# Kernel tuning notes

Hardware: AMD Instinct MI355X
Metric: run time of the kernel (lower is better)

Reference implementation:

```python
import jax, jax.numpy as jnp
import numpy as np

K_NEIGHBORS = 6
LN_EPS = 1e-5


def _layernorm(h, g, b):
    m = h.mean(-1, keepdims=True)
    v = h.var(-1, keepdims=True)
    return (h - m) / jnp.sqrt(v + LN_EPS) * g + b


def _mlp(h, w0, b0, w1, b1):
    return jax.nn.relu(h @ w0 + b0) @ w1 + b1


def _learn_adj(x, Wp, bp):
    # EfficientGraphStructureLearner: cosine-sim topk graph, symmetrized, row-normalized
    h = x @ Wp + bp
    nrm = jnp.linalg.norm(h, axis=1, keepdims=True)
    h = h / jnp.maximum(nrm, 1e-12)
    S = h @ h.T                                  # [N, N]
    vals, idx = jax.lax.top_k(S, K_NEIGHBORS + 1)  # col 0 is self (diag == 1)
    N = x.shape[0]
    rows = jnp.arange(N)[:, None]
    adj = jnp.zeros_like(S).at[rows, idx[:, 1:]].set(vals[:, 1:])
    adj = (adj + adj.T) * 0.5
    adj = adj / (adj.sum(1, keepdims=True) + 1e-8)
    return adj


def _gcn(h, adj, W, b):
    # StandardGraphConv: D^-1/2 (A+I) D^-1/2 @ (h W) + b (diag matmuls as row/col scaling)
    A = adj + jnp.eye(adj.shape[0], dtype=adj.dtype)
    d = jnp.maximum(A.sum(1), 1e-12) ** -0.5
    norm_adj = d[:, None] * A * d[None, :]
    return norm_adj @ (h @ W) + b


def setup_inputs() -> dict:
    key = jax.random.key(0)
    ks = iter(jax.random.split(key, 40))
    N, D, H, O, HP = 8192, 20, 32, 128, 16
    f = lambda *s: jax.random.normal(next(ks), s, dtype=jnp.float32) * 0.1
    inp = {
        'x': jax.random.normal(next(ks), (N, D), dtype=jnp.float32),
        'Wp': f(D, HP), 'bp': jnp.zeros((HP,), jnp.float32),
        'gw0': f(D, H), 'gb0': jnp.zeros((H,), jnp.float32),
        'gw1': f(H, H), 'gb1': jnp.zeros((H,), jnp.float32),
        'gw2': f(H, O), 'gb2': jnp.zeros((O,), jnp.float32),
        'lg0': jnp.ones((H,), jnp.float32), 'lb0': jnp.zeros((H,), jnp.float32),
        'lg1': jnp.ones((H,), jnp.float32), 'lb1': jnp.zeros((H,), jnp.float32),
        'lg2': jnp.ones((O,), jnp.float32), 'lb2': jnp.zeros((O,), jnp.float32),
        'riw0': f(D, H), 'rib0': jnp.zeros((H,), jnp.float32),
        'riw1': f(H, H), 'rib1': jnp.zeros((H,), jnp.float32),
        'rhw0': f(H, H), 'rhb0': jnp.zeros((H,), jnp.float32),
        'rhw1': f(H, H), 'rhb1': jnp.zeros((H,), jnp.float32),
        'row0': f(H, O), 'rob0': jnp.zeros((O,), jnp.float32),
        'row1': f(O, O), 'rob1': jnp.zeros((O,), jnp.float32),
    }
    return inp


def reference(x, Wp, bp, gw0, gb0, gw1, gb1, gw2, gb2,
              lg0, lb0, lg1, lb1, lg2, lb2,
              riw0, rib0, riw1, rib1,
              rhw0, rhb0, rhw1, rhb1,
              row0, rob0, row1, rob1):
    adj = _learn_adj(x, Wp, bp)
    gcns = [(gw0, gb0, lg0, lb0), (gw1, gb1, lg1, lb1), (gw2, gb2, lg2, lb2)]
    skips = [(riw0, rib0, riw1, rib1), (rhw0, rhb0, rhw1, rhb1), (row0, rob0, row1, rob1)]
    h = x
    for i, ((W, b, g, bt), sk) in enumerate(zip(gcns, skips)):
        h_new = jax.nn.relu(_layernorm(_gcn(h, adj, W, b), g, bt))
        h = h_new + _mlp(h, *sk)
        # dropout is identity in eval mode
    return h
```

## Files before the change

### kernel.cpp

```cpp
#include <hip/hip_runtime.h>

constexpr int D_IN = 20;
constexpr int HP   = 16;
constexpr int K    = 6;
constexpr int SAMP = 512;
constexpr int NC   = 8;
constexpr int CAPC = 192;
constexpr int CIN  = 128;
constexpr float MARGIN = 0.02f;

typedef __attribute__((ext_vector_type(8))) short bf16x8;
typedef __attribute__((ext_vector_type(4))) float f32x4;

__device__ __forceinline__ float dot16_seq(const float4* q, const float4* c) {
  float s = 0.f;
#pragma unroll
  for (int m = 0; m < 4; ++m) {
    s = fmaf(q[m].x, c[m].x, s);
    s = fmaf(q[m].y, c[m].y, s);
    s = fmaf(q[m].z, c[m].z, s);
    s = fmaf(q[m].w, c[m].w, s);
  }
  return s;
}

__device__ __forceinline__ short f2bf(float f) {
  unsigned u = __float_as_uint(f);
  unsigned r = (u + 0x7fffu + ((u >> 16) & 1u)) >> 16;
  return (short)r;
}

__device__ __forceinline__ float dinv_of(float own, float ins) {
  float rs = 0.5f * (own + ins);
  float rn = 1.f / (rs + 1e-8f);
  return rsqrtf(fmaxf(1.f + rs * rn, 1e-12f));
}

__global__ void k_proj(const float* __restrict__ x, const float* __restrict__ Wp,
                       const float* __restrict__ bp, const float* __restrict__ gw0,
                       float* __restrict__ hn, short* __restrict__ hnb,
                       float* __restrict__ XW0,
                       float* __restrict__ insum, int* __restrict__ indeg, int N) {
  int i = blockIdx.x * blockDim.x + threadIdx.x;
  if (i >= N) return;
  insum[i] = 0.f; indeg[i] = 0;
  float xr[D_IN];
#pragma unroll
  for (int d = 0; d < D_IN; ++d) xr[d] = x[i*D_IN + d];
  float hv[HP];
  float nrm2 = 0.f;
#pragma unroll
  for (int h = 0; h < HP; ++h) {
    float a = bp[h];
#pragma unroll
    for (int d = 0; d < D_IN; ++d) a += xr[d] * Wp[d*HP + h];
    hv[h] = a;
    nrm2 += a * a;
  }
  float inv = 1.f / fmaxf(sqrtf(nrm2), 1e-12f);
#pragma unroll
  for (int h = 0; h < HP; ++h) {
    float v = hv[h] * inv;
    hn[i*HP + h] = v;
    hnb[(size_t)i*32 + h] = f2bf(v);
  }
#pragma unroll
  for (int h = 0; h < HP; ++h) hnb[(size_t)i*32 + 16 + h] = 0;
#pragma unroll
  for (int oc = 0; oc < 32; ++oc) {
    float a = 0.f;
#pragma unroll
    for (int d = 0; d < D_IN; ++d) a += xr[d] * gw0[d*32 + oc];
    XW0[(size_t)i*32 + oc] = a;
  }
}

struct Top6 { float v0,v1,v2,v3,v4,v5; int i0,i1,i2,i3,i4,i5; };

__device__ __forceinline__ void t6_init(Top6& t) {
  t.v0=t.v1=t.v2=t.v3=t.v4=t.v5=-1e30f;
  t.i0=t.i1=t.i2=t.i3=t.i4=t.i5=-1;
}

#define T6_SWAP(a,b,ia,ib) { float tv=a; a=b; b=tv; int ti=ia; ia=ib; ib=ti; }

__device__ __forceinline__ void t6_insert(Top6& t, float s, int c) {
  if (s > t.v5) {
    t.v5 = s; t.i5 = c;
    if (t.v5 > t.v4) { T6_SWAP(t.v4, t.v5, t.i4, t.i5); }
    if (t.v4 > t.v3) { T6_SWAP(t.v3, t.v4, t.i3, t.i4); }
    if (t.v3 > t.v2) { T6_SWAP(t.v2, t.v3, t.i2, t.i3); }
    if (t.v2 > t.v1) { T6_SWAP(t.v1, t.v2, t.i1, t.i2); }
    if (t.v1 > t.v0) { T6_SWAP(t.v0, t.v1, t.i0, t.i1); }
  }
}

__device__ __forceinline__ void t6_best(const Top6& t, float& cv, int& ci) {
  cv = t.v0; ci = t.i0;
  if (t.v1 > cv || (t.v1 == cv && (unsigned)t.i1 < (unsigned)ci)) { cv = t.v1; ci = t.i1; }
  if (t.v2 > cv || (t.v2 == cv && (unsigned)t.i2 < (unsigned)ci)) { cv = t.v2; ci = t.i2; }
  if (t.v3 > cv || (t.v3 == cv && (unsigned)t.i3 < (unsigned)ci)) { cv = t.v3; ci = t.i3; }
  if (t.v4 > cv || (t.v4 == cv && (unsigned)t.i4 < (unsigned)ci)) { cv = t.v4; ci = t.i4; }
  if (t.v5 > cv || (t.v5 == cv && (unsigned)t.i5 < (unsigned)ci)) { cv = t.v5; ci = t.i5; }
}

__device__ __forceinline__ void t6_consume(Top6& t, int mi) {
  if (t.i0 == mi) t.v0 = -1e30f;
  if (t.i1 == mi) t.v1 = -1e30f;
  if (t.i2 == mi) t.v2 = -1e30f;
  if (t.i3 == mi) t.v3 = -1e30f;
  if (t.i4 == mi) t.v4 = -1e30f;
  if (t.i5 == mi) t.v5 = -1e30f;
}

__global__ __launch_bounds__(256) void k_thresh(const float* __restrict__ hn,
                                                float* __restrict__ tau, int N) {
  int wave = threadIdx.x >> 6, lane = threadIdx.x & 63;
  int row = blockIdx.x * 4 + wave;
  const float4* hn4 = (const float4*)hn;
  float4 q[4];
#pragma unroll
  for (int m = 0; m < 4; ++m) q[m] = hn4[(size_t)row*4 + m];
  Top6 t; t6_init(t);
#pragma unroll
  for (int k = 0; k < SAMP/64; ++k) {
    int c = lane + 64*k;
    if (c != row) {
      float4 cv[4];
#pragma unroll
      for (int m = 0; m < 4; ++m) cv[m] = hn4[(size_t)c*4 + m];
      float s = dot16_seq(q, cv);
      t6_insert(t, s, c);
    }
  }
  float last = -1e30f;
  for (int sel = 0; sel < K; ++sel) {
    float cv; int ci;
    t6_best(t, cv, ci);
    float mv = cv; int mi = ci;
#pragma unroll
    for (int m = 1; m < 64; m <<= 1) {
      float ov = __shfl_xor(mv, m);
      int   oi = __shfl_xor(mi, m);
      if (ov > mv || (ov == mv && (unsigned)oi < (unsigned)mi)) { mv = ov; mi = oi; }
    }
    t6_consume(t, mi);
    last = mv;
  }
  if (lane == 0) tau[row] = last;
}

__global__ __launch_bounds__(256) void k_scan2(
    const short* __restrict__ hnb, const float* __restrict__ tau,
    int* __restrict__ cnt, unsigned short* __restrict__ buf, int N) {
  __shared__ int cntl[16];
  int rb = blockIdx.x / NC;
  int jc = blockIdx.x % NC;
  int wave = threadIdx.x >> 6, lane = threadIdx.x & 63;
  int r0 = rb * 16;
  int half = lane >> 4;
  int l16  = lane & 15;

  if (threadIdx.x < 16) cntl[threadIdx.x] = 0;
  __syncthreads();

  bf16x8 a = *(const bf16x8*)(hnb + (size_t)(r0 + l16)*32 + half*8);
  float4 t4 = *(const float4*)(tau + r0 + half*4);
  float tm0 = t4.x - MARGIN, tm1 = t4.y - MARGIN,
        tm2 = t4.z - MARGIN, tm3 = t4.w - MARGIN;
  f32x4 zero = {0.f, 0.f, 0.f, 0.f};

  const int SPANW = N / NC / 4;
  int jb0 = jc * (N / NC) + wave * SPANW;

#define APPB(R, COND)                                                        \
  {                                                                          \
    unsigned long long mr = __ballot(COND);                                  \
    if (l16 == 0) {                                                          \
      unsigned mask = (unsigned)(mr >> (16*half)) & 0xFFFFu;                 \
      if (mask) {                                                            \
        int row = r0 + half*4 + (R);                                         \
        int pos = atomicAdd(&cntl[4*half + (R)], __popc(mask));              \
        unsigned mm = mask;                                                  \
        while (mm) {                                                         \
          int bx = __ffs(mm) - 1; mm &= mm - 1;                              \
          if (pos < CAPC)                                                    \
            buf[((size_t)row*NC + jc)*CAPC + pos] = (unsigned short)(jb + bx); \
          ++pos;                                                             \
        }                                                                    \
      }                                                                      \
    }                                                                        \
  }

#pragma unroll 4
  for (int jt = 0; jt < SPANW; jt += 16) {
    int jb = jb0 + jt;
    bf16x8 b = *(const bf16x8*)(hnb + (size_t)(jb + l16)*32 + half*8);
    f32x4 d = __builtin_amdgcn_mfma_f32_16x16x32_bf16(a, b, zero, 0, 0, 0);
    bool h0 = d[0] >= tm0, h1 = d[1] >= tm1, h2 = d[2] >= tm2, h3 = d[3] >= tm3;
    if (__any(h0 | h1 | h2 | h3)) {
      APPB(0, h0) APPB(1, h1) APPB(2, h2) APPB(3, h3)
    }
  }
#undef APPB

  __syncthreads();
  if (threadIdx.x < 16)
    cnt[(size_t)(r0 + threadIdx.x)*NC + jc] = min(cntl[threadIdx.x], CAPC);
}

__global__ __launch_bounds__(256) void k_final(
    const float* __restrict__ hn, const unsigned short* __restrict__ buf,
    const int* __restrict__ cnt,
    float* __restrict__ evals, int* __restrict__ eidx,
    float* __restrict__ ownsum, float* insum, int* indeg,
    unsigned short* __restrict__ incol, float* __restrict__ inval, int N) {
  int wave = threadIdx.x >> 6, lane = threadIdx.x & 63;
  int row = blockIdx.x * 4 + wave;
  const float4* hn4 = (const float4*)hn;
  float4 q[4];
#pragma unroll
  for (int m = 0; m < 4; ++m) q[m] = hn4[(size_t)row*4 + m];

  int cbase = row * NC;
  int cl = (lane < NC) ? cnt[cbase + lane] : 0;
  int c0 = __shfl(cl, 0), c1 = __shfl(cl, 1), c2 = __shfl(cl, 2), c3 = __shfl(cl, 3),
      c4 = __shfl(cl, 4), c5 = __shfl(cl, 5), c6 = __shfl(cl, 6), c7 = __shfl(cl, 7);
  int p1 = c0, p2 = p1 + c1, p3 = p2 + c2, p4 = p3 + c3,
      p5 = p4 + c4, p6 = p5 + c5, p7 = p6 + c6, T = p7 + c7;

  Top6 t; t6_init(t);
  for (int e = lane; e < T; e += 64) {
    int s, off;
    if (e < p4) {
      if (e < p2) { if (e < p1) { s = 0; off = e; } else { s = 1; off = e - p1; } }
      else        { if (e < p3) { s = 2; off = e - p2; } else { s = 3; off = e - p3; } }
    } else {
      if (e < p6) { if (e < p5) { s = 4; off = e - p4; } else { s = 5; off = e - p5; } }
      else        { if (e < p7) { s = 6; off = e - p6; } else { s = 7; off = e - p7; } }
    }
    int j = buf[((size_t)cbase + s)*CAPC + off];
    if (j != row) {
      float4 cv[4];
#pragma unroll
      for (int m = 0; m < 4; ++m) cv[m] = hn4[(size_t)j*4 + m];
      float sc = dot16_seq(q, cv);
      t6_insert(t, sc, j);
    }
  }
  float osum = 0.f;
  for (int sel = 0; sel < K; ++sel) {
    float cv; int ci;
    t6_best(t, cv, ci);
    float mv = cv; int mi = ci;
#pragma unroll
    for (int m = 1; m < 64; m <<= 1) {
      float ov = __shfl_xor(mv, m);
      int   oi = __shfl_xor(mi, m);
      if (ov > mv || (ov == mv && (unsigned)oi < (unsigned)mi)) { mv = ov; mi = oi; }
    }
    t6_consume(t, mi);
    if (lane == 0) {
      evals[row*K + sel] = mv;
      eidx [row*K + sel] = mi;
      osum += mv;
      atomicAdd(&insum[mi], mv);
      int pos = atomicAdd(&indeg[mi], 1);
      if (pos < CIN) {
        incol[(size_t)mi*CIN + pos] = (unsigned short)row;
        inval[(size_t)mi*CIN + pos] = mv;
      }
    }
  }
  if (lane == 0) ownsum[row] = osum;
}

template<int DIN, int NEXTD>
__global__ __launch_bounds__(256) void k_gpost32(
    const float* __restrict__ XWsrc,
    const int* __restrict__ eidx, const float* __restrict__ evals,
    const unsigned short* __restrict__ incol, const float* __restrict__ inval,
    const int* __restrict__ indeg,
    const float* __restrict__ ownsum, const float* __restrict__ insum,
    const float* __restrict__ gb, const float* __restrict__ lg, const float* __restrict__ lb,
    const float* __restrict__ hprev,
    const float* __restrict__ w0, const float* __restrict__ b0,
    const float* __restrict__ w1, const float* __restrict__ b1,
    const float* __restrict__ Wnext, float* __restrict__ XWnext,
    float* __restrict__ outp, int N) {
  __shared__ float hid[4][2][32];
  int tid = threadIdx.x;
  int lane = tid & 63, wslot = tid >> 6;
  int sub = lane >> 5, ol = lane & 31;
  int row = (blockIdx.x * 4 + wslot) * 2 + sub;

  float rs_i = 0.5f * (ownsum[row] + insum[row]);
  float rn_i = 1.f / (rs_i + 1e-8f);
  float di_i = rsqrtf(fmaxf(1.f + rs_i * rn_i, 1e-12f));
  float cc = 0.5f * di_i * rn_i;
  float acc = (di_i * di_i) * XWsrc[(size_t)row*32 + ol];
#pragma unroll
  for (int t = 0; t < K; ++t) {
    int j = eidx[row*K + t]; float v = evals[row*K + t];
    float dj = dinv_of(ownsum[j], insum[j]);
    acc = fmaf(cc * v * dj, XWsrc[(size_t)j*32 + ol], acc);
  }
  int ne = min(indeg[row], CIN);
  for (int e = 0; e < ne; ++e) {
    int j = incol[(size_t)row*CIN + e]; float v = inval[(size_t)row*CIN + e];
    float dj = dinv_of(ownsum[j], insum[j]);
    acc = fmaf(cc * v * dj, XWsrc[(size_t)j*32 + ol], acc);
  }
  float u0 = acc + gb[ol];
  float s = u0;
#pragma unroll
  for (int m = 1; m < 32; m <<= 1) s += __shfl_xor(s, m);
  float mean = s * (1.f/32.f);
  float d0 = u0 - mean;
  float vs = d0*d0;
#pragma unroll
  for (int m = 1; m < 32; m <<= 1) vs += __shfl_xor(vs, m);
  float rstd = rsqrtf(vs * (1.f/32.f) + 1e-5f);
  float t0 = fmaxf(d0*rstd*lg[ol] + lb[ol], 0.f);

  float hp[DIN];
#pragma unroll
  for (int d = 0; d < DIN; ++d) hp[d] = hprev[(size_t)row*DIN + d];
  float a = b0[ol];
#pragma unroll
  for (int d = 0; d < DIN; ++d) a = fmaf(hp[d], w0[d*32 + ol], a);
  hid[wslot][sub][ol] = fmaxf(a, 0.f);
  float o = b1[ol];
#pragma unroll
  for (int h = 0; h < 32; ++h) o = fmaf(hid[wslot][sub][h], w1[h*32 + ol], o);
  float hv = t0 + o;
  outp[(size_t)row*32 + ol] = hv;

  hid[wslot][sub][ol] = hv;
#pragma unroll
  for (int k2 = 0; k2 < NEXTD/32; ++k2) {
    int oc = ol + 32*k2;
    float acc2 = 0.f;
#pragma unroll
    for (int d = 0; d < 32; ++d)
      acc2 = fmaf(hid[wslot][sub][d], Wnext[d*NEXTD + oc], acc2);
    XWnext[(size_t)row*NEXTD + oc] = acc2;
  }
}

__global__ __launch_bounds__(256) void k_gpost128(
    const float* __restrict__ XW,
    const int* __restrict__ eidx, const float* __restrict__ evals,
    const unsigned short* __restrict__ incol, const float* __restrict__ inval,
    const int* __restrict__ indeg,
    const float* __restrict__ ownsum, const float* __restrict__ insum,
    const float* __restrict__ b, const float* __restrict__ g, const float* __restrict__ bt,
    const float* __restrict__ hprev,
    const float* __restrict__ w0, const float* __restrict__ b0,
    const float* __restrict__ w1, const float* __restrict__ b1,
    float* __restrict__ out, int N) {
  __shared__ float hid_s[4][128];
  __shared__ float w1s[2048];
  int wslot = threadIdx.x >> 6;
  int row   = (blockIdx.x * blockDim.x + threadIdx.x) >> 6;
  int lane  = threadIdx.x & 63;
  int o0 = lane, o1 = lane + 64;

  float rs_i = 0.5f * (ownsum[row] + insum[row]);
  float rn_i = 1.f / (rs_i + 1e-8f);
  float di_i = rsqrtf(fmaxf(1.f + rs_i * rn_i, 1e-12f));
  float cc = 0.5f * di_i * rn_i;
  float sc = di_i * di_i;
  float acc0 = sc * XW[(size_t)row*128 + o0];
  float acc1 = sc * XW[(size_t)row*128 + o1];
#pragma unroll
  for (int t = 0; t < K; ++t) {
    int j = eidx[row*K + t]; float v = evals[row*K + t];
    float dj = dinv_of(ownsum[j], insum[j]);
    float cf = cc * v * dj;
    acc0 = fmaf(cf, XW[(size_t)j*128 + o0], acc0);
    acc1 = fmaf(cf, XW[(size_t)j*128 + o1], acc1);
  }
  int ne = min(indeg[row], CIN);
  for (int e = 0; e < ne; ++e) {
    int j = incol[(size_t)row*CIN + e]; float v = inval[(size_t)row*CIN + e];
    float dj = dinv_of(ownsum[j], insum[j]);
    float cf = cc * v * dj;
    acc0 = fmaf(cf, XW[(size_t)j*128 + o0], acc0);
    acc1 = fmaf(cf, XW[(size_t)j*128 + o1], acc1);
  }
  float u0 = acc0 + b[o0];
  float u1 = acc1 + b[o1];

  float s = u0 + u1;
#pragma unroll
  for (int m = 1; m < 64; m <<= 1) s += __shfl_xor(s, m);
  float mean = s * (1.f/128.f);
  float d0 = u0 - mean, d1 = u1 - mean;
  float vs = d0*d0 + d1*d1;
#pragma unroll
  for (int m = 1; m < 64; m <<= 1) vs += __shfl_xor(vs, m);
  float rstd = rsqrtf(vs * (1.f/128.f) + 1e-5f);
  float t0 = fmaxf(d0*rstd*g[o0] + bt[o0], 0.f);
  float t1 = fmaxf(d1*rstd*g[o1] + bt[o1], 0.f);

  float hp[32];
#pragma unroll
  for (int d = 0; d < 32; ++d) hp[d] = hprev[(size_t)row*32 + d];
  {
    float a = b0[o0];
#pragma unroll
    for (int d = 0; d < 32; ++d) a = fmaf(hp[d], w0[d*128 + o0], a);
    hid_s[wslot][o0] = fmaxf(a, 0.f);
    float a1 = b0[o1];
#pragma unroll
    for (int d = 0; d < 32; ++d) a1 = fmaf(hp[d], w0[d*128 + o1], a1);
    hid_s[wslot][o1] = fmaxf(a1, 0.f);
  }

  float r0=0.f, r1=0.f, r2=0.f, r3=0.f, q0=0.f, q1=0.f, q2=0.f, q3=0.f;
  for (int c = 0; c < 8; ++c) {
    __syncthreads();
    {
      const float4* src = (const float4*)(w1 + c*2048);
      float4* dst = (float4*)w1s;
      dst[threadIdx.x]       = src[threadIdx.x];
      dst[threadIdx.x + 256] = src[threadIdx.x + 256];
    }
    __syncthreads();
    int hb = c*16;
#pragma unroll
    for (int hh = 0; hh < 16; hh += 4) {
      float h0 = hid_s[wslot][hb+hh+0], h1 = hid_s[wslot][hb+hh+1],
            h2 = hid_s[wslot][hb+hh+2], h3 = hid_s[wslot][hb+hh+3];
      r0 = fmaf(h0, w1s[(hh+0)*128 + o0], r0); q0 = fmaf(h0, w1s[(hh+0)*128 + o1], q0);
      r1 = fmaf(h1, w1s[(hh+1)*128 + o0], r1); q1 = fmaf(h1, w1s[(hh+1)*128 + o1], q1);
      r2 = fmaf(h2, w1s[(hh+2)*128 + o0], r2); q2 = fmaf(h2, w1s[(hh+2)*128 + o1], q2);
      r3 = fmaf(h3, w1s[(hh+3)*128 + o0], r3); q3 = fmaf(h3, w1s[(hh+3)*128 + o1], q3);
    }
  }
  out[(size_t)row*128 + o0] = t0 + b1[o0] + ((r0 + r1) + (r2 + r3));
  out[(size_t)row*128 + o1] = t1 + b1[o1] + ((q0 + q1) + (q2 + q3));
}

extern "C" void kernel_launch(void* const* d_in, const int* in_sizes, int n_in,
                              void* d_out, int out_size, void* d_ws, size_t ws_size,
                              hipStream_t stream) {
  const float* x    = (const float*)d_in[0];
  const float* Wp   = (const float*)d_in[1];
  const float* bp   = (const float*)d_in[2];
  const float* gw0  = (const float*)d_in[3];
  const float* gb0  = (const float*)d_in[4];
  const float* gw1  = (const float*)d_in[5];
  const float* gb1  = (const float*)d_in[6];
  const float* gw2  = (const float*)d_in[7];
  const float* gb2  = (const float*)d_in[8];
  const float* lg0  = (const float*)d_in[9];
  const float* lb0  = (const float*)d_in[10];
  const float* lg1  = (const float*)d_in[11];
  const float* lb1  = (const float*)d_in[12];
  const float* lg2  = (const float*)d_in[13];
  const float* lb2  = (const float*)d_in[14];
  const float* riw0 = (const float*)d_in[15];
  const float* rib0 = (const float*)d_in[16];
  const float* riw1 = (const float*)d_in[17];
  const float* rib1 = (const float*)d_in[18];
  const float* rhw0 = (const float*)d_in[19];
  const float* rhb0 = (const float*)d_in[20];
  const float* rhw1 = (const float*)d_in[21];
  const float* rhb1 = (const float*)d_in[22];
  const float* row0 = (const float*)d_in[23];
  const float* rob0 = (const float*)d_in[24];
  const float* row1 = (const float*)d_in[25];
  const float* rob1 = (const float*)d_in[26];
  int N = in_sizes[0] / D_IN;
  float* out = (float*)d_out;

  char* ws = (char*)d_ws;
  size_t off = 0;
  auto alloc = [&](size_t bytes) -> void* {
    void* p = ws + off;
    off += (bytes + 255) & ~(size_t)255;
    return p;
  };
  float* hn      = (float*)alloc((size_t)N * HP * 4);
  float* evals   = (float*)alloc((size_t)N * K * 4);
  int*   eidx    = (int*)  alloc((size_t)N * K * 4);
  float* ownsum  = (float*)alloc((size_t)N * 4);
  float* insum   = (float*)alloc((size_t)N * 4);
  int*   indeg   = (int*)  alloc((size_t)N * 4);
  float* XWa     = (float*)alloc((size_t)N * 128 * 4);
  float* XWb     = (float*)alloc((size_t)N * 32 * 4);
  float* h1      = (float*)alloc((size_t)N * 32 * 4);
  float* h2      = (float*)alloc((size_t)N * 32 * 4);
  float* tau     = (float*)alloc((size_t)N * 4);
  int*   cnt     = (int*)  alloc((size_t)N * NC * 4);
  unsigned short* buf = (unsigned short*)alloc((size_t)N * NC * CAPC * 2);
  short* hnb     = (short*)alloc((size_t)N * 32 * 2);
  unsigned short* incol = (unsigned short*)alloc((size_t)N * CIN * 2);
  float* inval   = (float*)alloc((size_t)N * CIN * 4);
  (void)ws_size; (void)n_in; (void)out_size;

  const int B = 256;
  hipLaunchKernelGGL(k_proj, dim3((N + B - 1) / B), dim3(B), 0, stream,
                     x, Wp, bp, gw0, hn, hnb, XWa, insum, indeg, N);
  hipLaunchKernelGGL(k_thresh, dim3(N / 4), dim3(B), 0, stream, hn, tau, N);
  hipLaunchKernelGGL(k_scan2, dim3((N / 16) * NC), dim3(B), 0, stream, hnb, tau, cnt, buf, N);
  hipLaunchKernelGGL(k_final, dim3(N / 4), dim3(B), 0, stream,
                     hn, buf, cnt, evals, eidx, ownsum, insum, indeg, incol, inval, N);

  hipLaunchKernelGGL((k_gpost32<20, 32>), dim3(N / 8), dim3(B), 0, stream,
                     XWa, eidx, evals, incol, inval, indeg, ownsum, insum,
                     gb0, lg0, lb0, x, riw0, rib0, riw1, rib1, gw1, XWb, h1, N);
  hipLaunchKernelGGL((k_gpost32<32, 128>), dim3(N / 8), dim3(B), 0, stream,
                     XWb, eidx, evals, incol, inval, indeg, ownsum, insum,
                     gb1, lg1, lb1, h1, rhw0, rhb0, rhw1, rhb1, gw2, XWa, h2, N);
  hipLaunchKernelGGL(k_gpost128, dim3(N / 4), dim3(B), 0, stream,
                     XWa, eidx, evals, incol, inval, indeg, ownsum, insum,
                     gb2, lg2, lb2, h2, row0, rob0, row1, rob1, out, N);
}
```

Measured before the change: 153.9 us.

## Fuse threshold sampling into projection kernel and pre-scale XW by degree

The separate threshold kernel is folded into the projection kernel. Each thread now computes its 6th-best cosine similarity against the 256 rows of its own block, read from shared memory, instead of a wave-wide top-6 over 512 sampled rows, which removes one launch and a global reload of hn. Separately, each row's XW output is pre-multiplied by its own D^-1/2 factor, so the second and third GCN aggregations no longer gather ownsum and insum for every neighbour. The threshold sample changes (its own block's 256 rows instead of the first 512 rows, and per-thread instead of per-wave), which may shift the candidate counts in the scan buffers and their overflow behaviour.

```diff
diff --git a/kernel.cpp b/kernel.cpp
--- a/kernel.cpp
+++ b/kernel.cpp
@@ -3,7 +3,6 @@
 constexpr int D_IN = 20;
 constexpr int HP   = 16;
 constexpr int K    = 6;
-constexpr int SAMP = 512;
 constexpr int NC   = 8;
 constexpr int CAPC = 192;
 constexpr int CIN  = 128;
@@ -34,45 +33,6 @@
   float rs = 0.5f * (own + ins);
   float rn = 1.f / (rs + 1e-8f);
   return rsqrtf(fmaxf(1.f + rs * rn, 1e-12f));
-}
-
-__global__ void k_proj(const float* __restrict__ x, const float* __restrict__ Wp,
-                       const float* __restrict__ bp, const float* __restrict__ gw0,
-                       float* __restrict__ hn, short* __restrict__ hnb,
-                       float* __restrict__ XW0,
-                       float* __restrict__ insum, int* __restrict__ indeg, int N) {
-  int i = blockIdx.x * blockDim.x + threadIdx.x;
-  if (i >= N) return;
-  insum[i] = 0.f; indeg[i] = 0;
-  float xr[D_IN];
-#pragma unroll
-  for (int d = 0; d < D_IN; ++d) xr[d] = x[i*D_IN + d];
-  float hv[HP];
-  float nrm2 = 0.f;
-#pragma unroll
-  for (int h = 0; h < HP; ++h) {
-    float a = bp[h];
-#pragma unroll
-    for (int d = 0; d < D_IN; ++d) a += xr[d] * Wp[d*HP + h];
-    hv[h] = a;
-    nrm2 += a * a;
-  }
-  float inv = 1.f / fmaxf(sqrtf(nrm2), 1e-12f);
-#pragma unroll
-  for (int h = 0; h < HP; ++h) {
-    float v = hv[h] * inv;
-    hn[i*HP + h] = v;
-    hnb[(size_t)i*32 + h] = f2bf(v);
-  }
-#pragma unroll
-  for (int h = 0; h < HP; ++h) hnb[(size_t)i*32 + 16 + h] = 0;
-#pragma unroll
-  for (int oc = 0; oc < 32; ++oc) {
-    float a = 0.f;
-#pragma unroll
-    for (int d = 0; d < D_IN; ++d) a += xr[d] * gw0[d*32 + oc];
-    XW0[(size_t)i*32 + oc] = a;
-  }
 }
 
 struct Top6 { float v0,v1,v2,v3,v4,v5; int i0,i1,i2,i3,i4,i5; };
@@ -113,41 +73,63 @@
   if (t.i5 == mi) t.v5 = -1e30f;
 }
 
-__global__ __launch_bounds__(256) void k_thresh(const float* __restrict__ hn,
-                                                float* __restrict__ tau, int N) {
-  int wave = threadIdx.x >> 6, lane = threadIdx.x & 63;
-  int row = blockIdx.x * 4 + wave;
-  const float4* hn4 = (const float4*)hn;
+__global__ __launch_bounds__(256) void k_proj(
+    const float* __restrict__ x, const float* __restrict__ Wp,
+    const float* __restrict__ bp, const float* __restrict__ gw0,
+    float* __restrict__ hn, short* __restrict__ hnb,
+    float* __restrict__ XW0, float* __restrict__ tau,
+    float* __restrict__ insum, int* __restrict__ indeg, int N) {
+  __shared__ float hs[256][20];
+  int tid = threadIdx.x;
+  int i = blockIdx.x * 256 + tid;
+  insum[i] = 0.f; indeg[i] = 0;
+  float xr[D_IN];
+#pragma unroll
+  for (int d = 0; d < D_IN; ++d) xr[d] = x[i*D_IN + d];
+  float hv[HP];
+  float nrm2 = 0.f;
+#pragma unroll
+  for (int h = 0; h < HP; ++h) {
+    float a = bp[h];
+#pragma unroll
+    for (int d = 0; d < D_IN; ++d) a += xr[d] * Wp[d*HP + h];
+    hv[h] = a;
+    nrm2 += a * a;
+  }
+  float inv = 1.f / fmaxf(sqrtf(nrm2), 1e-12f);
+#pragma unroll
+  for (int h = 0; h < HP; ++h) {
+    float v = hv[h] * inv;
+    hv[h] = v;
+    hn[i*HP + h] = v;
+    hnb[(size_t)i*32 + h] = f2bf(v);
+    hs[tid][h] = v;
+  }
+#pragma unroll
+  for (int h = 0; h < HP; ++h) hnb[(size_t)i*32 + 16 + h] = 0;
+#pragma unroll
+  for (int oc = 0; oc < 32; ++oc) {
+    float a = 0.f;
+#pragma unroll
+    for (int d = 0; d < D_IN; ++d) a += xr[d] * gw0[d*32 + oc];
+    XW0[(size_t)i*32 + oc] = a;
+  }
+  __syncthreads();
+
   float4 q[4];
 #pragma unroll
-  for (int m = 0; m < 4; ++m) q[m] = hn4[(size_t)row*4 + m];
+  for (int m = 0; m < 4; ++m)
+    q[m] = make_float4(hv[4*m+0], hv[4*m+1], hv[4*m+2], hv[4*m+3]);
   Top6 t; t6_init(t);
-#pragma unroll
-  for (int k = 0; k < SAMP/64; ++k) {
-    int c = lane + 64*k;
-    if (c != row) {
-      float4 cv[4];
-#pragma unroll
-      for (int m = 0; m < 4; ++m) cv[m] = hn4[(size_t)c*4 + m];
-      float s = dot16_seq(q, cv);
-      t6_insert(t, s, c);
-    }
-  }
-  float last = -1e30f;
-  for (int sel = 0; sel < K; ++sel) {
-    float cv; int ci;
-    t6_best(t, cv, ci);
-    float mv = cv; int mi = ci;
-#pragma unroll
-    for (int m = 1; m < 64; m <<= 1) {
-      float ov = __shfl_xor(mv, m);
-      int   oi = __shfl_xor(mi, m);
-      if (ov > mv || (ov == mv && (unsigned)oi < (unsigned)mi)) { mv = ov; mi = oi; }
-    }
-    t6_consume(t, mi);
-    last = mv;
-  }
-  if (lane == 0) tau[row] = last;
+#pragma unroll 4
+  for (int c = 0; c < 256; ++c) {
+    float4 cv[4];
+#pragma unroll
+    for (int m = 0; m < 4; ++m) cv[m] = *(const float4*)&hs[c][4*m];
+    float s = dot16_seq(q, cv);
+    if (c != tid) t6_insert(t, s, c);
+  }
+  tau[i] = t.v5;
 }
 
 __global__ __launch_bounds__(256) void k_scan2(
@@ -275,7 +257,7 @@
   if (lane == 0) ownsum[row] = osum;
 }
 
-template<int DIN, int NEXTD>
+template<int DIN, int NEXTD, bool SCALED>
 __global__ __launch_bounds__(256) void k_gpost32(
     const float* __restrict__ XWsrc,
     const int* __restrict__ eidx, const float* __restrict__ evals,
@@ -298,18 +280,22 @@
   float rn_i = 1.f / (rs_i + 1e-8f);
   float di_i = rsqrtf(fmaxf(1.f + rs_i * rn_i, 1e-12f));
   float cc = 0.5f * di_i * rn_i;
-  float acc = (di_i * di_i) * XWsrc[(size_t)row*32 + ol];
+  float acc = (SCALED ? di_i : di_i * di_i) * XWsrc[(size_t)row*32 + ol];
 #pragma unroll
   for (int t = 0; t < K; ++t) {
     int j = eidx[row*K + t]; float v = evals[row*K + t];
-    float dj = dinv_of(ownsum[j], insum[j]);
-    acc = fmaf(cc * v * dj, XWsrc[(size_t)j*32 + ol], acc);
+    float cf;
+    if constexpr (SCALED) cf = cc * v;
+    else                  cf = cc * v * dinv_of(ownsum[j], insum[j]);
+    acc = fmaf(cf, XWsrc[(size_t)j*32 + ol], acc);
   }
   int ne = min(indeg[row], CIN);
   for (int e = 0; e < ne; ++e) {
     int j = incol[(size_t)row*CIN + e]; float v = inval[(size_t)row*CIN + e];
-    float dj = dinv_of(ownsum[j], insum[j]);
-    acc = fmaf(cc * v * dj, XWsrc[(size_t)j*32 + ol], acc);
+    float cf;
+    if constexpr (SCALED) cf = cc * v;
+    else                  cf = cc * v * dinv_of(ownsum[j], insum[j]);
+    acc = fmaf(cf, XWsrc[(size_t)j*32 + ol], acc);
   }
   float u0 = acc + gb[ol];
   float s = u0;
@@ -344,7 +330,7 @@
 #pragma unroll
     for (int d = 0; d < 32; ++d)
       acc2 = fmaf(hid[wslot][sub][d], Wnext[d*NEXTD + oc], acc2);
-    XWnext[(size_t)row*NEXTD + oc] = acc2;
+    XWnext[(size_t)row*NEXTD + oc] = di_i * acc2;
   }
 }
 
@@ -370,22 +356,19 @@
   float rn_i = 1.f / (rs_i + 1e-8f);
   float di_i = rsqrtf(fmaxf(1.f + rs_i * rn_i, 1e-12f));
   float cc = 0.5f * di_i * rn_i;
-  float sc = di_i * di_i;
-  float acc0 = sc * XW[(size_t)row*128 + o0];
-  float acc1 = sc * XW[(size_t)row*128 + o1];
+  float acc0 = di_i * XW[(size_t)row*128 + o0];
+  float acc1 = di_i * XW[(size_t)row*128 + o1];
 #pragma unroll
   for (int t = 0; t < K; ++t) {
-    int j = eidx[row*K + t]; float v = evals[row*K + t];
-    float dj = dinv_of(ownsum[j], insum[j]);
-    float cf = cc * v * dj;
+    int j = eidx[row*K + t];
+    float cf = cc * evals[row*K + t];
     acc0 = fmaf(cf, XW[(size_t)j*128 + o0], acc0);
     acc1 = fmaf(cf, XW[(size_t)j*128 + o1], acc1);
   }
   int ne = min(indeg[row], CIN);
   for (int e = 0; e < ne; ++e) {
-    int j = incol[(size_t)row*CIN + e]; float v = inval[(size_t)row*CIN + e];
-    float dj = dinv_of(ownsum[j], insum[j]);
-    float cf = cc * v * dj;
+    int j = incol[(size_t)row*CIN + e];
+    float cf = cc * inval[(size_t)row*CIN + e];
     acc0 = fmaf(cf, XW[(size_t)j*128 + o0], acc0);
     acc1 = fmaf(cf, XW[(size_t)j*128 + o1], acc1);
   }
@@ -502,17 +485,16 @@
   (void)ws_size; (void)n_in; (void)out_size;
 
   const int B = 256;
-  hipLaunchKernelGGL(k_proj, dim3((N + B - 1) / B), dim3(B), 0, stream,
-                     x, Wp, bp, gw0, hn, hnb, XWa, insum, indeg, N);
-  hipLaunchKernelGGL(k_thresh, dim3(N / 4), dim3(B), 0, stream, hn, tau, N);
+  hipLaunchKernelGGL(k_proj, dim3(N / 256), dim3(256), 0, stream,
+                     x, Wp, bp, gw0, hn, hnb, XWa, tau, insum, indeg, N);
   hipLaunchKernelGGL(k_scan2, dim3((N / 16) * NC), dim3(B), 0, stream, hnb, tau, cnt, buf, N);
   hipLaunchKernelGGL(k_final, dim3(N / 4), dim3(B), 0, stream,
                      hn, buf, cnt, evals, eidx, ownsum, insum, indeg, incol, inval, N);
 
-  hipLaunchKernelGGL((k_gpost32<20, 32>), dim3(N / 8), dim3(B), 0, stream,
+  hipLaunchKernelGGL((k_gpost32<20, 32, false>), dim3(N / 8), dim3(B), 0, stream,
                      XWa, eidx, evals, incol, inval, indeg, ownsum, insum,
                      gb0, lg0, lb0, x, riw0, rib0, riw1, rib1, gw1, XWb, h1, N);
-  hipLaunchKernelGGL((k_gpost32<32, 128>), dim3(N / 8), dim3(B), 0, stream,
+  hipLaunchKernelGGL((k_gpost32<32, 128, true>), dim3(N / 8), dim3(B), 0, stream,
                      XWb, eidx, evals, incol, inval, indeg, ownsum, insum,
                      gb1, lg1, lb1, h1, rhw0, rhb0, rhw1, rhb1, gw2, XWa, h2, N);
   hipLaunchKernelGGL(k_gpost128, dim3(N / 4), dim3(B), 0, stream,
```

Measured after the change: 179.8 us. 16.8% more time.
